# Kernel tuning notes

Hardware: AMD Instinct MI355X
Metric: run time of the kernel (lower is better)

Reference implementation:

```python
import jax, jax.numpy as jnp
import numpy as np

NUM_EMBEDDINGS = 1024
EMBEDDING_DIM = 64
COMMITMENT_COST = 0.25
EPSILON = 1e-10


def setup_inputs() -> dict:
    key = jax.random.key(0)
    k1, k2 = jax.random.split(key)
    z_e = jax.random.normal(k1, (32, EMBEDDING_DIM, 64, 64), dtype=jnp.float32)
    # torch init: uniform(-1/K, 1/K)
    lim = 1.0 / NUM_EMBEDDINGS
    embedding = jax.random.uniform(k2, (NUM_EMBEDDINGS, EMBEDDING_DIM),
                                   dtype=jnp.float32, minval=-lim, maxval=lim)
    return {"z_e": z_e, "embedding": embedding}


def reference(z_e, embedding):
    # NCHW -> NHWC
    z = jnp.transpose(z_e, (0, 2, 3, 1))  # [B,H,W,D]
    input_shape = z.shape
    flat = z.reshape(-1, EMBEDDING_DIM)  # [N,D]

    x2 = jnp.sum(flat ** 2, axis=1, keepdims=True)          # [N,1]
    e2 = jnp.sum(embedding ** 2, axis=1)                     # [K]
    ip = jnp.matmul(flat, embedding.T)                       # [N,K]
    distances = x2 + e2 - 2.0 * ip

    encoding_indices = jnp.argmin(distances, axis=1)         # [N]
    encodings = jax.nn.one_hot(encoding_indices, NUM_EMBEDDINGS,
                               dtype=jnp.float32)            # [N,K]

    z_q = jnp.matmul(encodings, embedding).reshape(input_shape)  # [B,H,W,D]

    commitment_loss = COMMITMENT_COST * jnp.mean((jax.lax.stop_gradient(z_q) - z) ** 2)
    e2z_loss = jnp.mean((z_q - jax.lax.stop_gradient(z)) ** 2)
    vq_loss = commitment_loss + e2z_loss

    # straight-through estimator
    z_q = z + jax.lax.stop_gradient(z_q - z)

    avg_probs = jnp.mean(encodings, axis=0)  # [K]
    perplexity = jnp.exp(-jnp.sum(avg_probs * jnp.log(avg_probs + EPSILON)))

    z_q_out = jnp.transpose(z_q, (0, 3, 1, 2))  # back to NCHW
    return (vq_loss, z_q_out, perplexity, encodings)
```

## Files before the change

### kernel.cpp

```cpp
#include <hip/hip_runtime.h>
#include <cfloat>
#include <stdint.h>


typedef __attribute__((ext_vector_type(8))) short bf8v;
typedef __attribute__((ext_vector_type(4))) float f4v;

__device__ __forceinline__ unsigned short f2bf(float v) {
  unsigned u = __float_as_uint(v);
  return (unsigned short)((u + 0x7FFFu + ((u >> 16) & 1u)) >> 16);
}
__device__ __forceinline__ float bf2f(unsigned short h) {
  return __uint_as_float(((unsigned)h) << 16);
}

__global__ __launch_bounds__(256) void vq_prep(const float* __restrict__ emb,
                                               float* __restrict__ ws) {
  #pragma clang fp contract(off)
  int gid = blockIdx.x * 256 + threadIdx.x;
  if (gid == 0) ws[0] = 0.0f;
  ((int*)ws)[1 + gid] = 0;
  const float* e = emb + (gid << 6);
  float r[8];
  #pragma unroll
  for (int j = 0; j < 8; ++j) r[j] = e[j] * e[j];
  #pragma unroll
  for (int i = 8; i < 64; i += 8) {
    #pragma unroll
    for (int j = 0; j < 8; ++j) { float s = e[i + j] * e[i + j]; r[j] = r[j] + s; }
  }
  ws[1025 + gid] = ((r[0] + r[1]) + (r[2] + r[3])) + ((r[4] + r[5]) + (r[6] + r[7]));
}

__global__ __launch_bounds__(256) void vq_prep_frags(const float* __restrict__ emb,
                                                     float* __restrict__ out) {
  int e = blockIdx.x * 256 + threadIdx.x;
  int lane = e & 63, sub = e >> 6;
  int term = sub % 3, kk = (sub / 3) & 1, nt = sub / 6;
  int code = nt * 16 + (lane & 15);
  int d0 = kk * 32 + (lane >> 4) * 8;
  const float* src = emb + code * 64 + d0;
  unsigned short hs[8];
  #pragma unroll
  for (int j = 0; j < 8; ++j) {
    float v = src[j];
    unsigned short h = f2bf(v);  float r1 = v - bf2f(h);
    unsigned short m = f2bf(r1); float r2 = r1 - bf2f(m);
    unsigned short l = f2bf(r2);
    hs[j] = (term == 0) ? h : (term == 1) ? m : l;
  }
  uint4 p;
  p.x = (unsigned)hs[0] | ((unsigned)hs[1] << 16);
  p.y = (unsigned)hs[2] | ((unsigned)hs[3] << 16);
  p.z = (unsigned)hs[4] | ((unsigned)hs[5] << 16);
  p.w = (unsigned)hs[6] | ((unsigned)hs[7] << 16);
  ((uint4*)(out + 4))[e] = p;
}

__global__ __launch_bounds__(256, 4) void vq_main(const float* __restrict__ ze,
                                                  float* __restrict__ ws,
                                                  float* __restrict__ out) {
  __shared__ float xtile[64 * 68];
  __shared__ __align__(16) short bbuf[2 * 6 * 64 * 8];
  __shared__ float e2s[1024];
  __shared__ float x2s[64];
  __shared__ float sx[256];

  int t = threadIdx.x;
  int w = __builtin_amdgcn_readfirstlane(t >> 6);
  int lane = t & 63;
  int g = blockIdx.x;
  int b = g >> 6, h = g & 63;
  int n0 = g << 6;

  const float* zebase = ze + ((size_t)b << 18) + (h << 6);
  #pragma unroll
  for (int i = 0; i < 16; ++i) {
    int d = w * 16 + i;
    xtile[lane * 68 + d] = zebase[d * 4096 + lane];
  }
  e2s[t] = ws[1025 + t];         e2s[256 + t] = ws[1281 + t];
  e2s[512 + t] = ws[1537 + t];   e2s[768 + t] = ws[1793 + t];
  __syncthreads();

  {
    #pragma clang fp contract(off)
    const float* xr = xtile + lane * 68;
    int j0 = 2 * w, j1 = 2 * w + 1;
    float v0 = xr[j0], v1 = xr[j1];
    float ra = v0 * v0, rb = v1 * v1;
    #pragma unroll
    for (int p = 1; p < 8; ++p) {
      float s0 = xr[8 * p + j0]; s0 = s0 * s0; ra = ra + s0;
      float s1 = xr[8 * p + j1]; s1 = s1 * s1; rb = rb + s1;
    }
    sx[lane * 4 + w] = ra + rb;
  }
  __syncthreads();
  if (t < 64) x2s[t] = (sx[t * 4] + sx[t * 4 + 1]) + (sx[t * 4 + 2] + sx[t * 4 + 3]);
  __syncthreads();

  int qd = lane >> 4, rr = lane & 15;
  const float* xr = xtile + (w * 16 + rr) * 68;
  bf8v Ah[2], Am[2], Al[2];
  #pragma unroll
  for (int kk = 0; kk < 2; ++kk) {
    #pragma unroll
    for (int j = 0; j < 8; ++j) {
      float v = xr[kk * 32 + qd * 8 + j];
      unsigned short hh = f2bf(v);  float r1 = v - bf2f(hh);
      unsigned short mm = f2bf(r1); float r2 = r1 - bf2f(mm);
      unsigned short ll = f2bf(r2);
      Ah[kk][j] = (short)hh; Am[kk][j] = (short)mm; Al[kk][j] = (short)ll;
    }
  }
  float x2v[4];
  #pragma unroll
  for (int r = 0; r < 4; ++r) x2v[r] = x2s[w * 16 + qd * 4 + r];

  const uint4* ft = (const uint4*)(out + 4);
  uint4* bput = (uint4*)bbuf;
  float* encbase = out + 8388610 + (size_t)n0 * 1024;
  const float2 z2 = make_float2(0.0f, 0.0f);

  for (int f = w; f < 6; f += 4) bput[f * 64 + lane] = ft[f * 64 + lane];
  __syncthreads();

  unsigned long long best[4] = {~0ULL, ~0ULL, ~0ULL, ~0ULL};

  #pragma unroll 1
  for (int nt = 0; nt < 64; ++nt) {
    int cur = nt & 1, nxt = cur ^ 1;
    uint4 pv0, pv1;
    if (nt < 63) {
      pv0 = ft[((nt + 1) * 6 + w) * 64 + lane];
      if (w < 2) pv1 = ft[((nt + 1) * 6 + w + 4) * 64 + lane];
    }
    float e2v = e2s[nt * 16 + (lane & 15)];
    f4v acc = {0.0f, 0.0f, 0.0f, 0.0f};
    const bf8v* bb = (const bf8v*)bbuf + cur * 6 * 64;
    #pragma unroll
    for (int kk = 0; kk < 2; ++kk) {
      bf8v Bh = bb[(kk * 3 + 0) * 64 + lane];
      bf8v Bm = bb[(kk * 3 + 1) * 64 + lane];
      bf8v Bl = bb[(kk * 3 + 2) * 64 + lane];
      acc = __builtin_amdgcn_mfma_f32_16x16x32_bf16(Ah[kk], Bh, acc, 0, 0, 0);
      acc = __builtin_amdgcn_mfma_f32_16x16x32_bf16(Ah[kk], Bm, acc, 0, 0, 0);
      acc = __builtin_amdgcn_mfma_f32_16x16x32_bf16(Am[kk], Bh, acc, 0, 0, 0);
      acc = __builtin_amdgcn_mfma_f32_16x16x32_bf16(Am[kk], Bm, acc, 0, 0, 0);
      acc = __builtin_amdgcn_mfma_f32_16x16x32_bf16(Ah[kk], Bl, acc, 0, 0, 0);
      acc = __builtin_amdgcn_mfma_f32_16x16x32_bf16(Al[kk], Bh, acc, 0, 0, 0);
    }
    unsigned code0 = (unsigned)(nt * 16 + (lane & 15));
    #pragma unroll
    for (int r = 0; r < 4; ++r) {
      float tt = x2v[r] + e2v;
      float dd = fmaf(-2.0f, acc[r], tt);
      unsigned long long cand =
          (((unsigned long long)__float_as_uint(dd)) << 32) | code0;
      if (cand < best[r]) best[r] = cand;
    }
    float2* ez = (float2*)(encbase + nt * 1024) + t;
    ez[0] = z2; ez[256] = z2;
    if (nt < 63) {
      bput[(nxt * 6 + w) * 64 + lane] = pv0;
      if (w < 2) bput[(nxt * 6 + w + 4) * 64 + lane] = pv1;
    }
    __syncthreads();
  }

  #pragma unroll
  for (int r = 0; r < 4; ++r) {
    unsigned long long bu = best[r];
    #pragma unroll
    for (int m = 1; m <= 8; m <<= 1) {
      unsigned long long o = __shfl_xor(bu, m, 64);
      if (o < bu) bu = o;
    }
    best[r] = bu;
  }
  if ((lane & 15) == 0) {
    #pragma unroll
    for (int r = 0; r < 4; ++r)
      ((int*)encbase)[w * 16 + qd * 4 + r] = (int)(best[r] & 0xFFFFFFFFu);
  }
}

__global__ __launch_bounds__(256) void vq_out(const float* __restrict__ ze,
                                              const float* __restrict__ emb,
                                              float* __restrict__ ws,
                                              float* __restrict__ out) {
  __shared__ float red[4];
  int g = blockIdx.x, t = threadIdx.x;
  int b = g >> 6, h = g & 63, n0 = g << 6;
  float* enc = out + 8388610;
  int* wp = (int*)(enc + (size_t)n0 * 1024);
  int row = t & 63;
  int gi = wp[row];
  __syncthreads();
  if (t < 64) ((float*)wp)[t] = 0.0f;
  __syncthreads();
  if (t < 64) enc[(size_t)(n0 + t) * 1024 + gi] = 1.0f;

  const float* er = emb + gi * 64;
  const float* zr = ze + ((size_t)b << 18) + (h << 6) + row;
  float* qr = out + 1 + ((size_t)b << 18) + (h << 6) + row;
  float ls = 0.0f;
  #pragma unroll
  for (int i = 0; i < 16; ++i) {
    int d = (t >> 6) * 16 + i;
    float v = er[d];
    float df = v - zr[(size_t)d * 4096];
    ls = fmaf(df, df, ls);
    qr[(size_t)d * 4096] = v;
  }
  #pragma unroll
  for (int off = 32; off > 0; off >>= 1) ls += __shfl_down(ls, off, 64);
  if ((t & 63) == 0) red[t >> 6] = ls;
  __syncthreads();
  if (t == 0) atomicAdd(ws, (red[0] + red[1]) + (red[2] + red[3]));
  if (t < 64) atomicAdd((int*)ws + 1 + gi, 1);
}

__global__ __launch_bounds__(1024) void vq_fin(const float* __restrict__ ws,
                                               float* __restrict__ out) {
  __shared__ float sm[16];
  int t = threadIdx.x;
  const int* counts = (const int*)ws + 1;
  float c = (float)counts[t];
  float p = c * (1.0f / 131072.0f);
  float s = p * logf(p + 1e-10f);
  #pragma unroll
  for (int off = 32; off > 0; off >>= 1) s += __shfl_down(s, off, 64);
  if ((t & 63) == 0) sm[t >> 6] = s;
  __syncthreads();
  if (t == 0) {
    float v = 0.0f;
    #pragma unroll
    for (int i = 0; i < 16; ++i) v += sm[i];
    out[8388609] = expf(-v);
    float m = ws[0] / 8388608.0f;
    out[0] = 0.25f * m + m;
  }
}

extern "C" void kernel_launch(void* const* d_in, const int* in_sizes, int n_in,
                              void* d_out, int out_size, void* d_ws, size_t ws_size,
                              hipStream_t stream) {
  const float* ze  = (const float*)d_in[0];
  const float* emb = (const float*)d_in[1];
  float* out = (float*)d_out;
  float* ws  = (float*)d_ws;
  vq_prep<<<4, 256, 0, stream>>>(emb, ws);
  vq_prep_frags<<<96, 256, 0, stream>>>(emb, out);
  vq_main<<<2048, 256, 0, stream>>>(ze, ws, out);
  vq_out<<<2048, 256, 0, stream>>>(ze, emb, ws, out);
  vq_fin<<<1, 1024, 0, stream>>>(ws, out);
}
```

Measured before the change: 666.2 us.

## Load codebook B-fragments directly from global into registers, drop LDS staging

Each wave now loads its bf16 split codebook fragments straight from global memory (expected to hit L2) into registers, double-buffered across two unrolled register sets. This removes the shared-memory double buffer and the per-tile __syncthreads. The aim is to cut LDS traffic and barrier stalls in the distance loop. In exchange, every wave loads all six fragments itself instead of sharing them (4x the global/L2 reads), and register pressure rises. A barrier is added before the index write so no wave writes into encbase while another may still be writing zeros there.

```diff
diff --git a/kernel.cpp b/kernel.cpp
--- a/kernel.cpp
+++ b/kernel.cpp
@@ -57,11 +57,44 @@
   ((uint4*)(out + 4))[e] = p;
 }
 
+#define LOADB(P, ntv) do {                                        \
+    const bf8v* _p = fp0 + (ntv) * 384;                           \
+    P##0 = _p[0];   P##1 = _p[64];  P##2 = _p[128];               \
+    P##3 = _p[192]; P##4 = _p[256]; P##5 = _p[320];               \
+  } while (0)
+
+#define STEPB(P, ntv) do {                                                       \
+    float e2v = e2s[(ntv) * 16 + (lane & 15)];                                   \
+    f4v acc = {0.0f, 0.0f, 0.0f, 0.0f};                                          \
+    acc = __builtin_amdgcn_mfma_f32_16x16x32_bf16(Ah[0], P##0, acc, 0, 0, 0);    \
+    acc = __builtin_amdgcn_mfma_f32_16x16x32_bf16(Ah[0], P##1, acc, 0, 0, 0);    \
+    acc = __builtin_amdgcn_mfma_f32_16x16x32_bf16(Am[0], P##0, acc, 0, 0, 0);    \
+    acc = __builtin_amdgcn_mfma_f32_16x16x32_bf16(Am[0], P##1, acc, 0, 0, 0);    \
+    acc = __builtin_amdgcn_mfma_f32_16x16x32_bf16(Ah[0], P##2, acc, 0, 0, 0);    \
+    acc = __builtin_amdgcn_mfma_f32_16x16x32_bf16(Al[0], P##0, acc, 0, 0, 0);    \
+    acc = __builtin_amdgcn_mfma_f32_16x16x32_bf16(Ah[1], P##3, acc, 0, 0, 0);    \
+    acc = __builtin_amdgcn_mfma_f32_16x16x32_bf16(Ah[1], P##4, acc, 0, 0, 0);    \
+    acc = __builtin_amdgcn_mfma_f32_16x16x32_bf16(Am[1], P##3, acc, 0, 0, 0);    \
+    acc = __builtin_amdgcn_mfma_f32_16x16x32_bf16(Am[1], P##4, acc, 0, 0, 0);    \
+    acc = __builtin_amdgcn_mfma_f32_16x16x32_bf16(Ah[1], P##5, acc, 0, 0, 0);    \
+    acc = __builtin_amdgcn_mfma_f32_16x16x32_bf16(Al[1], P##3, acc, 0, 0, 0);    \
+    unsigned code0 = (unsigned)((ntv) * 16 + (lane & 15));                       \
+    _Pragma("unroll")                                                            \
+    for (int r = 0; r < 4; ++r) {                                                \
+      float tt = x2v[r] + e2v;                         \
+      float dd = fmaf(-2.0f, acc[r], tt);                \
+      unsigned long long cand =                                                  \
+          (((unsigned long long)__float_as_uint(dd)) << 32) | code0;             \
+      if (cand < best[r]) best[r] = cand;               \
+    }                                                                            \
+    float2* ez = (float2*)(encbase + (ntv) * 1024) + t;                          \
+    ez[0] = z2; ez[256] = z2;                                                    \
+  } while (0)
+
 __global__ __launch_bounds__(256, 4) void vq_main(const float* __restrict__ ze,
                                                   float* __restrict__ ws,
                                                   float* __restrict__ out) {
   __shared__ float xtile[64 * 68];
-  __shared__ __align__(16) short bbuf[2 * 6 * 64 * 8];
   __shared__ float e2s[1024];
   __shared__ float x2s[64];
   __shared__ float sx[256];
@@ -118,55 +151,21 @@
   #pragma unroll
   for (int r = 0; r < 4; ++r) x2v[r] = x2s[w * 16 + qd * 4 + r];
 
-  const uint4* ft = (const uint4*)(out + 4);
-  uint4* bput = (uint4*)bbuf;
+  const bf8v* fp0 = (const bf8v*)(out + 4) + lane;
   float* encbase = out + 8388610 + (size_t)n0 * 1024;
   const float2 z2 = make_float2(0.0f, 0.0f);
 
-  for (int f = w; f < 6; f += 4) bput[f * 64 + lane] = ft[f * 64 + lane];
-  __syncthreads();
-
   unsigned long long best[4] = {~0ULL, ~0ULL, ~0ULL, ~0ULL};
 
+  bf8v Xa0, Xa1, Xa2, Xa3, Xa4, Xa5;
+  bf8v Xb0, Xb1, Xb2, Xb3, Xb4, Xb5;
+  LOADB(Xa, 0);
   #pragma unroll 1
-  for (int nt = 0; nt < 64; ++nt) {
-    int cur = nt & 1, nxt = cur ^ 1;
-    uint4 pv0, pv1;
-    if (nt < 63) {
-      pv0 = ft[((nt + 1) * 6 + w) * 64 + lane];
-      if (w < 2) pv1 = ft[((nt + 1) * 6 + w + 4) * 64 + lane];
-    }
-    float e2v = e2s[nt * 16 + (lane & 15)];
-    f4v acc = {0.0f, 0.0f, 0.0f, 0.0f};
-    const bf8v* bb = (const bf8v*)bbuf + cur * 6 * 64;
-    #pragma unroll
-    for (int kk = 0; kk < 2; ++kk) {
-      bf8v Bh = bb[(kk * 3 + 0) * 64 + lane];
-      bf8v Bm = bb[(kk * 3 + 1) * 64 + lane];
-      bf8v Bl = bb[(kk * 3 + 2) * 64 + lane];
-      acc = __builtin_amdgcn_mfma_f32_16x16x32_bf16(Ah[kk], Bh, acc, 0, 0, 0);
-      acc = __builtin_amdgcn_mfma_f32_16x16x32_bf16(Ah[kk], Bm, acc, 0, 0, 0);
-      acc = __builtin_amdgcn_mfma_f32_16x16x32_bf16(Am[kk], Bh, acc, 0, 0, 0);
-      acc = __builtin_amdgcn_mfma_f32_16x16x32_bf16(Am[kk], Bm, acc, 0, 0, 0);
-      acc = __builtin_amdgcn_mfma_f32_16x16x32_bf16(Ah[kk], Bl, acc, 0, 0, 0);
-      acc = __builtin_amdgcn_mfma_f32_16x16x32_bf16(Al[kk], Bh, acc, 0, 0, 0);
-    }
-    unsigned code0 = (unsigned)(nt * 16 + (lane & 15));
-    #pragma unroll
-    for (int r = 0; r < 4; ++r) {
-      float tt = x2v[r] + e2v;
-      float dd = fmaf(-2.0f, acc[r], tt);
-      unsigned long long cand =
-          (((unsigned long long)__float_as_uint(dd)) << 32) | code0;
-      if (cand < best[r]) best[r] = cand;
-    }
-    float2* ez = (float2*)(encbase + nt * 1024) + t;
-    ez[0] = z2; ez[256] = z2;
-    if (nt < 63) {
-      bput[(nxt * 6 + w) * 64 + lane] = pv0;
-      if (w < 2) bput[(nxt * 6 + w + 4) * 64 + lane] = pv1;
-    }
-    __syncthreads();
+  for (int nt = 0; nt < 64; nt += 2) {
+    LOADB(Xb, nt + 1);
+    STEPB(Xa, nt);
+    if (nt < 62) LOADB(Xa, nt + 2);
+    STEPB(Xb, nt + 1);
   }
 
   #pragma unroll
@@ -179,6 +178,7 @@
     }
     best[r] = bu;
   }
+  __syncthreads();
   if ((lane & 15) == 0) {
     #pragma unroll
     for (int r = 0; r < 4; ++r)
```

After: 745.5 us. 11.9% more time.

## Fuse output epilogue into main VQ kernel for most batches

Applied to the files above, without the earlier changes.

Moves the one-hot write, histogram atomics, z_q gather/write and loss accumulation into the tail of vq_main for batches 1..31, using the x tile already held in shared memory. vq_out now runs only 64 blocks to handle batch 0, whose encoding rows still hold the fragment data that must be cleared first. This removes a second full pass that re-read z_e and the index workspace, at the cost of more work and registers in the main kernel's epilogue.

```diff
diff --git a/kernel.cpp b/kernel.cpp
--- a/kernel.cpp
+++ b/kernel.cpp
@@ -58,6 +58,7 @@
 }
 
 __global__ __launch_bounds__(256, 4) void vq_main(const float* __restrict__ ze,
+                                                  const float* __restrict__ emb,
                                                   float* __restrict__ ws,
                                                   float* __restrict__ out) {
   __shared__ float xtile[64 * 68];
@@ -65,6 +66,8 @@
   __shared__ float e2s[1024];
   __shared__ float x2s[64];
   __shared__ float sx[256];
+  __shared__ int warr[64];
+  __shared__ float red[4];
 
   int t = threadIdx.x;
   int w = __builtin_amdgcn_readfirstlane(t >> 6);
@@ -179,10 +182,49 @@
     }
     best[r] = bu;
   }
+
+  if (b == 0) {
+    if ((lane & 15) == 0) {
+      #pragma unroll
+      for (int r = 0; r < 4; ++r)
+        ((int*)encbase)[w * 16 + qd * 4 + r] = (int)(best[r] & 0xFFFFFFFFu);
+    }
+    return;
+  }
+
   if ((lane & 15) == 0) {
     #pragma unroll
     for (int r = 0; r < 4; ++r)
-      ((int*)encbase)[w * 16 + qd * 4 + r] = (int)(best[r] & 0xFFFFFFFFu);
+      warr[w * 16 + qd * 4 + r] = (int)(best[r] & 0xFFFFFFFFu);
+  }
+  __syncthreads();
+
+  if (t < 64) {
+    int gi = warr[t];
+    encbase[(size_t)t * 1024 + gi] = 1.0f;
+    atomicAdd((int*)ws + 1 + gi, 1);
+  }
+
+  {
+    int row = t & 63;
+    int gi = warr[row];
+    const float* er = emb + (gi << 6);
+    const float* xz = xtile + row * 68;
+    float* qr = out + 1 + ((size_t)b << 18) + (h << 6) + row;
+    float ls = 0.0f;
+    #pragma unroll
+    for (int i = 0; i < 16; ++i) {
+      int d = (t >> 6) * 16 + i;
+      float v = er[d];
+      float df = v - xz[d];
+      ls = fmaf(df, df, ls);
+      qr[(size_t)d * 4096] = v;
+    }
+    #pragma unroll
+    for (int off = 32; off > 0; off >>= 1) ls += __shfl_down(ls, off, 64);
+    if ((t & 63) == 0) red[t >> 6] = ls;
+    __syncthreads();
+    if (t == 0) atomicAdd(ws, (red[0] + red[1]) + (red[2] + red[3]));
   }
 }
 
@@ -253,7 +295,7 @@
   float* ws  = (float*)d_ws;
   vq_prep<<<4, 256, 0, stream>>>(emb, ws);
   vq_prep_frags<<<96, 256, 0, stream>>>(emb, out);
-  vq_main<<<2048, 256, 0, stream>>>(ze, ws, out);
-  vq_out<<<2048, 256, 0, stream>>>(ze, emb, ws, out);
+  vq_main<<<2048, 256, 0, stream>>>(ze, emb, ws, out);
+  vq_out<<<64, 256, 0, stream>>>(ze, emb, ws, out);
   vq_fin<<<1, 1024, 0, stream>>>(ws, out);
 }
```

New measurement: 641.5 us. 1.04x faster.
